# Optimization experiments

Measured on AMD Instinct MI355X. Metric: run time of the kernel, lower is better.

## Reference

```python
import jax, jax.numpy as jnp
import numpy as np

N_IMAGES = 2  # matches init kwarg


def setup_inputs() -> dict:
    key = jax.random.key(0)
    x = jax.random.normal(key, (8192, 128), dtype=jnp.float32)
    return {"x": x}


def reference(x):
    n_images = N_IMAGES
    N, D = x.shape
    P = N // n_images  # number of 'persons'
    G = x @ x.T  # [N, N] pairwise dot products (Gram matrix)

    # Offset pairs (i<j) within a window of n_images consecutive indices.
    # NB: original code uses range(person, person + n_images) -> sliding window.
    offs = np.array([(i, j) for i in range(n_images) for j in range(i + 1, n_images)])
    oi = jnp.asarray(offs[:, 0])  # [k]
    oj = jnp.asarray(offs[:, 1])  # [k]
    k = offs.shape[0]  # C(n_images, 2)

    p = jnp.arange(P)
    self_i = p[:, None] + oi[None, :]  # [P, k]
    self_j = p[:, None] + oj[None, :]  # [P, k]
    sim_self = jnp.min(G[self_i, self_j], axis=1)  # [P] min over self pairs

    # Upper-triangular (i<j) values; mask everything else to -inf.
    neg = jnp.finfo(G.dtype).min
    rows = jnp.arange(N)
    upper = jnp.where(rows[:, None] < rows[None, :], G, neg)

    # similarity_oth[p] = max over all i<j pairs excluding person p's k self pairs.
    # Only the global top-(k+1) values can ever be that max.
    top_vals, top_idx = jax.lax.top_k(upper.reshape(-1), k + 1)  # [k+1]
    self_flat = self_i * N + self_j  # [P, k] flat indices of self pairs
    member = (top_idx[None, :, None] == self_flat[:, None, :]).any(-1)  # [P, k+1]
    sim_oth = jnp.max(jnp.where(member, neg, top_vals[None, :]), axis=1)  # [P]

    return jnp.mean(sim_oth / sim_self)
```

## Files before the change

### kernel.cpp

```cpp
#include <hip/hip_runtime.h>
#include <hip/hip_bf16.h>
#include <math.h>
#include <float.h>

static constexpr int NN   = 8192;
static constexpr int DD   = 128;
static constexpr int PP   = 4096;
static constexpr int TT   = 64;
static constexpr int NBLK = TT * (TT + 1) / 2;
static constexpr int NC   = NBLK * 2;

struct Cand { float v; unsigned idx; };

using short8 = __attribute__((ext_vector_type(8))) short;
using f32x4  = __attribute__((ext_vector_type(4))) float;

__device__ __forceinline__ unsigned pk2(float lo, float hi) {
    unsigned a = (unsigned)__builtin_bit_cast(unsigned short, __float2bfloat16(lo));
    unsigned b = (unsigned)__builtin_bit_cast(unsigned short, __float2bfloat16(hi));
    return a | (b << 16);
}

__device__ __forceinline__ void push1(float& v1, unsigned& i1, float& v2, unsigned& i2,
                                      float w, unsigned j) {
    if (w > v1) { v2 = v1; i2 = i1; v1 = w; i1 = j; }
    else if (w > v2) { v2 = w; i2 = j; }
}

__device__ __forceinline__ void merge2(float& v1, unsigned& i1, float& v2, unsigned& i2,
                                       float w1, unsigned j1, float w2, unsigned j2) {
    if (w1 > v1) {
        float nv2; unsigned ni2;
        if (v1 >= w2) { nv2 = v1; ni2 = i1; } else { nv2 = w2; ni2 = j2; }
        v1 = w1; i1 = j1; v2 = nv2; i2 = ni2;
    } else if (w1 > v2) {
        v2 = w1; i2 = j1;
    }
}

__global__ __launch_bounds__(256) void k_prep(const float* __restrict__ x,
                                              char* __restrict__ xq,
                                              double* __restrict__ ss) {
    const int tid = threadIdx.x;
    if (blockIdx.x < 512) {
        int gg   = blockIdx.x * 256 + tid;
        int grp  = gg >> 8;
        int c    = (gg >> 4) & 15;
        int rloc = gg & 15;
        int r    = grp * 16 + rloc;
        const float4* s = (const float4*)(x + (size_t)r * DD + c * 8);
        float4 f0 = s[0], f1 = s[1];
        uint4 o = {pk2(f0.x, f0.y), pk2(f0.z, f0.w), pk2(f1.x, f1.y), pk2(f1.z, f1.w)};
        *(uint4*)(xq + (size_t)gg * 16) = o;
    } else {
        int b = blockIdx.x - 512;
        const int wv = tid >> 6, lane = tid & 63;
        #pragma unroll 4
        for (int u = 0; u < 16; ++u) {
            int p = b * 64 + wv * 16 + u;
            const float* a  = x + (size_t)p * DD;
            const float* bb = a + DD;
            double s = (double)a[lane] * (double)bb[lane]
                     + (double)a[lane + 64] * (double)bb[lane + 64];
            #pragma unroll
            for (int off = 32; off >= 1; off >>= 1) s += __shfl_down(s, off);
            if (lane == 0) ss[p] = s;
        }
    }
}

__global__ __launch_bounds__(256, 4) void k_top2(const char* __restrict__ xq,
                                                 Cand* __restrict__ cands) {
    __shared__ float sv1[4], sv2[4];
    __shared__ unsigned si1[4], si2[4];

    int rem = blockIdx.x;
    int ti = 0;
    while (rem >= TT - ti) { rem -= (TT - ti); ++ti; }
    int tj = ti + rem;

    const int tid  = threadIdx.x;
    const int wv   = tid >> 6;
    const int lane = tid & 63;
    const int quad = lane >> 4;
    const int r16  = lane & 15;
    const int wm   = wv >> 1;
    const int wn   = wv & 1;

    const char* fb = xq + (size_t)lane * 16;
    const int jg = tj * 8 + wn * 4;
    const int ig = ti * 8 + wm * 4;

    short8 bf[4][4];
    #pragma unroll
    for (int gn = 0; gn < 4; ++gn)
        #pragma unroll
        for (int s = 0; s < 4; ++s)
            bf[gn][s] = *(const short8*)(fb + (size_t)(jg + gn) * 4096 + s * 1024);

    float v1 = -INFINITY, v2 = -INFINITY;
    unsigned i1 = 0, i2 = 0;

    short8 am[4], an[4];
    #pragma unroll
    for (int s = 0; s < 4; ++s)
        am[s] = *(const short8*)(fb + (size_t)ig * 4096 + s * 1024);

    #pragma unroll
    for (int gm = 0; gm < 4; ++gm) {
        if (gm < 3) {
            #pragma unroll
            for (int s = 0; s < 4; ++s)
                an[s] = *(const short8*)(fb + (size_t)(ig + gm + 1) * 4096 + s * 1024);
        }
        #pragma unroll
        for (int gn = 0; gn < 4; ++gn) {
            f32x4 a = __builtin_amdgcn_mfma_f32_16x16x32_bf16(
                am[0], bf[gn][0], (f32x4){0.f, 0.f, 0.f, 0.f}, 0, 0, 0);
            #pragma unroll
            for (int s = 1; s < 4; ++s)
                a = __builtin_amdgcn_mfma_f32_16x16x32_bf16(
                    am[s], bf[gn][s], a, 0, 0, 0);
            int gj  = (jg + gn) * 16 + r16;
            int gib = (ig + gm) * 16 + quad * 4;
            #pragma unroll
            for (int reg = 0; reg < 4; ++reg) {
                int gi = gib + reg;
                if (gi < gj)
                    push1(v1, i1, v2, i2, a[reg], (unsigned)(gi * NN + gj));
            }
        }
        #pragma unroll
        for (int s = 0; s < 4; ++s) am[s] = an[s];
    }

    #pragma unroll
    for (int off = 32; off >= 1; off >>= 1) {
        float    w1 = __shfl_down(v1, off);
        unsigned j1 = (unsigned)__shfl_down((int)i1, off);
        float    w2 = __shfl_down(v2, off);
        unsigned j2 = (unsigned)__shfl_down((int)i2, off);
        merge2(v1, i1, v2, i2, w1, j1, w2, j2);
    }
    if (lane == 0) { sv1[wv] = v1; si1[wv] = i1; sv2[wv] = v2; si2[wv] = i2; }
    __syncthreads();
    if (tid == 0) {
        for (int w = 1; w < 4; ++w)
            merge2(v1, i1, v2, i2, sv1[w], si1[w], sv2[w], si2[w]);
        cands[blockIdx.x * 2]     = {v1, i1};
        cands[blockIdx.x * 2 + 1] = {v2, i2};
    }
}

__global__ __launch_bounds__(256) void k_final(const float* __restrict__ x,
                                               const double* __restrict__ ss,
                                               const Cand* __restrict__ cands,
                                               float* __restrict__ out) {
    __shared__ float redv[8];
    __shared__ float s_thresh;
    __shared__ int cnt;
    __shared__ unsigned qidx[128];
    __shared__ double qex[128];
    __shared__ double sd1, sd2;
    __shared__ unsigned stopi;
    __shared__ double sacc[256];

    const int tid  = threadIdx.x;
    const int wv   = tid >> 6;
    const int lane = tid & 63;
    if (tid == 0) cnt = 0;

    float v1 = -INFINITY, v2 = -INFINITY;
    for (int e = tid; e < NC; e += 256) {
        float v = cands[e].v;
        if (v > v1) { v2 = v1; v1 = v; }
        else if (v > v2) v2 = v;
    }
    #pragma unroll
    for (int off = 32; off >= 1; off >>= 1) {
        float w1 = __shfl_down(v1, off);
        float w2 = __shfl_down(v2, off);
        if (w1 > v1) { v2 = (v1 >= w2) ? v1 : w2; v1 = w1; }
        else if (w1 > v2) v2 = w1;
    }
    if (lane == 0) { redv[wv * 2] = v1; redv[wv * 2 + 1] = v2; }
    __syncthreads();
    if (tid == 0) {
        float a1 = -INFINITY, a2 = -INFINITY;
        for (int e = 0; e < 8; ++e) {
            float v = redv[e];
            if (v > a1) { a2 = a1; a1 = v; }
            else if (v > a2) a2 = v;
        }
        s_thresh = a2 - 1.0f;
    }
    __syncthreads();
    const float thresh = s_thresh;

    for (int e = tid; e < NC; e += 256) {
        if (cands[e].v >= thresh) {
            int k = atomicAdd(&cnt, 1);
            if (k < 128) qidx[k] = cands[e].idx;
        }
    }
    __syncthreads();
    const int n = cnt < 128 ? cnt : 128;

    for (int c = wv; c < n; c += 4) {
        unsigned idx = qidx[c];
        unsigned gi = idx >> 13;
        unsigned gj = idx & 8191;
        const float* pa = x + (size_t)gi * DD;
        const float* pb = x + (size_t)gj * DD;
        double s = (double)pa[lane] * (double)pb[lane]
                 + (double)pa[lane + 64] * (double)pb[lane + 64];
        #pragma unroll
        for (int off = 32; off >= 1; off >>= 1) s += __shfl_down(s, off);
        if (lane == 0) qex[c] = s;
    }
    __syncthreads();

    if (tid == 0) {
        double d1 = -DBL_MAX, d2 = -DBL_MAX;
        unsigned bi = 0;
        for (int c = 0; c < n; ++c) {
            double v = qex[c];
            if (v > d1) { d2 = d1; d1 = v; bi = qidx[c]; }
            else if (v > d2) d2 = v;
        }
        sd1 = d1; sd2 = d2; stopi = bi;
    }
    __syncthreads();

    const double top1 = sd1, top2 = sd2;
    const unsigned topi = stopi;

    double acc = 0.0;
    for (int p = tid; p < PP; p += 256) {
        unsigned selfidx = (unsigned)(p * NN + p + 1);
        double so = (topi == selfidx) ? top2 : top1;
        acc += so / ss[p];
    }
    sacc[tid] = acc;
    __syncthreads();
    for (int s = 128; s >= 1; s >>= 1) {
        if (tid < s) sacc[tid] += sacc[tid + s];
        __syncthreads();
    }
    if (tid == 0) out[0] = (float)(sacc[0] / (double)PP);
}

extern "C" void kernel_launch(void* const* d_in, const int* in_sizes, int n_in,
                              void* d_out, int out_size, void* d_ws, size_t ws_size,
                              hipStream_t stream) {
    (void)in_sizes; (void)n_in; (void)out_size; (void)ws_size;
    const float* x = (const float*)d_in[0];
    float* out = (float*)d_out;

    double* ss  = (double*)d_ws;
    Cand* cands = (Cand*)((char*)d_ws + 32768);
    char* xq    = (char*)d_ws + 131072;

    k_prep<<<576, 256, 0, stream>>>(x, xq, ss);
    k_top2<<<NBLK, 256, 0, stream>>>(xq, cands);
    k_final<<<1, 256, 0, stream>>>(x, ss, cands, out);
}
```

Measured before the change: 176.7 us.

## Enlarge k_top2 tiles to 256x256 with LDS-staged operands and 16 waves

Each k_top2 block now covers a 256x256 tile of the Gram matrix instead of 128x128, using 1024 threads (16 waves in a 4x4 layout). The A and B row panels are first copied cooperatively into 128 KB of shared memory, and the waves then read their MFMA fragments from LDS instead of global memory. This cuts the number of blocks and the redundant global and L2 fragment loads. In exchange it adds a block-wide barrier before compute and lowers occupancy: one large block per CU with 128 KB of LDS, and only 528 blocks across the GPU.

```diff
diff --git a/kernel.cpp b/kernel.cpp
--- a/kernel.cpp
+++ b/kernel.cpp
@@ -6,7 +6,7 @@
 static constexpr int NN   = 8192;
 static constexpr int DD   = 128;
 static constexpr int PP   = 4096;
-static constexpr int TT   = 64;
+static constexpr int TT   = 32;
 static constexpr int NBLK = TT * (TT + 1) / 2;
 static constexpr int NC   = NBLK * 2;
 
@@ -69,10 +69,12 @@
     }
 }
 
-__global__ __launch_bounds__(256, 4) void k_top2(const char* __restrict__ xq,
-                                                 Cand* __restrict__ cands) {
-    __shared__ float sv1[4], sv2[4];
-    __shared__ unsigned si1[4], si2[4];
+__global__ __launch_bounds__(1024) void k_top2(const char* __restrict__ xq,
+                                               Cand* __restrict__ cands) {
+    __shared__ __align__(16) char AsB[65536];
+    __shared__ __align__(16) char BsB[65536];
+    __shared__ float sv1[16], sv2[16];
+    __shared__ unsigned si1[16], si2[16];
 
     int rem = blockIdx.x;
     int ti = 0;
@@ -84,45 +86,50 @@
     const int lane = tid & 63;
     const int quad = lane >> 4;
     const int r16  = lane & 15;
-    const int wm   = wv >> 1;
-    const int wn   = wv & 1;
-
-    const char* fb = xq + (size_t)lane * 16;
-    const int jg = tj * 8 + wn * 4;
-    const int ig = ti * 8 + wm * 4;
+    const int wm   = wv >> 2;
+    const int wn   = wv & 3;
+
+    #pragma unroll
+    for (int t = 0; t < 8; ++t) {
+        int ch  = wv * 8 + t;
+        int isB = ch >> 6;
+        int c   = ch & 63;
+        const char* src = xq + ((size_t)((isB ? tj : ti) * 16) * 4096)
+                        + (size_t)c * 1024 + (size_t)lane * 16;
+        short8 d = *(const short8*)src;
+        char* dst = (isB ? BsB : AsB) + c * 1024 + lane * 16;
+        *(short8*)dst = d;
+    }
+    __syncthreads();
 
     short8 bf[4][4];
     #pragma unroll
     for (int gn = 0; gn < 4; ++gn)
         #pragma unroll
         for (int s = 0; s < 4; ++s)
-            bf[gn][s] = *(const short8*)(fb + (size_t)(jg + gn) * 4096 + s * 1024);
+            bf[gn][s] = *(const short8*)(BsB + (wn * 4 + gn) * 4096
+                                         + s * 1024 + lane * 16);
 
     float v1 = -INFINITY, v2 = -INFINITY;
     unsigned i1 = 0, i2 = 0;
 
-    short8 am[4], an[4];
-    #pragma unroll
-    for (int s = 0; s < 4; ++s)
-        am[s] = *(const short8*)(fb + (size_t)ig * 4096 + s * 1024);
-
     #pragma unroll
     for (int gm = 0; gm < 4; ++gm) {
-        if (gm < 3) {
-            #pragma unroll
-            for (int s = 0; s < 4; ++s)
-                an[s] = *(const short8*)(fb + (size_t)(ig + gm + 1) * 4096 + s * 1024);
-        }
+        short8 af[4];
+        #pragma unroll
+        for (int s = 0; s < 4; ++s)
+            af[s] = *(const short8*)(AsB + (wm * 4 + gm) * 4096
+                                     + s * 1024 + lane * 16);
         #pragma unroll
         for (int gn = 0; gn < 4; ++gn) {
             f32x4 a = __builtin_amdgcn_mfma_f32_16x16x32_bf16(
-                am[0], bf[gn][0], (f32x4){0.f, 0.f, 0.f, 0.f}, 0, 0, 0);
+                af[0], bf[gn][0], (f32x4){0.f, 0.f, 0.f, 0.f}, 0, 0, 0);
             #pragma unroll
             for (int s = 1; s < 4; ++s)
                 a = __builtin_amdgcn_mfma_f32_16x16x32_bf16(
-                    am[s], bf[gn][s], a, 0, 0, 0);
-            int gj  = (jg + gn) * 16 + r16;
-            int gib = (ig + gm) * 16 + quad * 4;
+                    af[s], bf[gn][s], a, 0, 0, 0);
+            int gj  = tj * 256 + (wn * 4 + gn) * 16 + r16;
+            int gib = ti * 256 + (wm * 4 + gm) * 16 + quad * 4;
             #pragma unroll
             for (int reg = 0; reg < 4; ++reg) {
                 int gi = gib + reg;
@@ -130,8 +137,6 @@
                     push1(v1, i1, v2, i2, a[reg], (unsigned)(gi * NN + gj));
             }
         }
-        #pragma unroll
-        for (int s = 0; s < 4; ++s) am[s] = an[s];
     }
 
     #pragma unroll
@@ -145,7 +150,7 @@
     if (lane == 0) { sv1[wv] = v1; si1[wv] = i1; sv2[wv] = v2; si2[wv] = i2; }
     __syncthreads();
     if (tid == 0) {
-        for (int w = 1; w < 4; ++w)
+        for (int w = 1; w < 16; ++w)
             merge2(v1, i1, v2, i2, sv1[w], si1[w], sv2[w], si2[w]);
         cands[blockIdx.x * 2]     = {v1, i1};
         cands[blockIdx.x * 2 + 1] = {v2, i2};
@@ -262,6 +267,6 @@
     char* xq    = (char*)d_ws + 131072;
 
     k_prep<<<576, 256, 0, stream>>>(x, xq, ss);
-    k_top2<<<NBLK, 256, 0, stream>>>(xq, cands);
+    k_top2<<<NBLK, 1024, 0, stream>>>(xq, cands);
     k_final<<<1, 256, 0, stream>>>(x, ss, cands, out);
 }
```

Result: slower. 187.8 us (+6.2%).
